# Kernel tuning notes

Hardware: AMD Instinct MI355X
Metric: run time of the kernel (lower is better)

## Reference

```python
import jax, jax.numpy as jnp
import numpy as np

B, S, D, I, L, H, F = 4, 512, 768, 64, 2, 12, 3072
DH = D // H
LN_EPS = 1e-12


def setup_inputs() -> dict:
    key = jax.random.key(0)
    ks = jax.random.split(key, 24)
    nrm = lambda k, sh, s=0.02: jax.random.normal(k, sh, jnp.float32) * s
    return {
        'hs0': nrm(ks[0], (B, S, D), 1.0),
        'hs1': nrm(ks[1], (B, S, D), 1.0),
        'hs2': nrm(ks[2], (B, S, D), 1.0),
        'Wq': nrm(ks[3], (L, D, D)), 'bq': jnp.zeros((L, D), jnp.float32),
        'Wk': nrm(ks[4], (L, D, D)), 'bk': jnp.zeros((L, D), jnp.float32),
        'Wv': nrm(ks[5], (L, D, D)), 'bv': jnp.zeros((L, D), jnp.float32),
        'Wo': nrm(ks[6], (L, D, D)), 'bo': jnp.zeros((L, D), jnp.float32),
        'ln1_g': jnp.ones((L, D), jnp.float32), 'ln1_b': jnp.zeros((L, D), jnp.float32),
        'W1': nrm(ks[7], (L, D, F)), 'b1': jnp.zeros((L, F), jnp.float32),
        'W2': nrm(ks[8], (L, F, D)), 'b2': jnp.zeros((L, D), jnp.float32),
        'ln2_g': jnp.ones((L, D), jnp.float32), 'ln2_b': jnp.zeros((L, D), jnp.float32),
        'zero_context': nrm(ks[9], (D,), 1.0),
        'ck2tok_mask': jax.random.uniform(ks[10], (B, I, S)) > 0.7,  # True = token excluded from span
        'span_size_ids': jax.random.randint(ks[11], (B, I), 0, 10),
    }


def _ln(x, g, b):
    m = jnp.mean(x, axis=-1, keepdims=True)
    v = jnp.mean((x - m) ** 2, axis=-1, keepdims=True)
    return (x - m) * jax.lax.rsqrt(v + LN_EPS) * g + b


def _forward(hs0, hs1, Wq, bq, Wk, bk, Wv, bv, Wo, bo, ln1_g, ln1_b,
             W1, b1, W2, b2, ln2_g, ln2_b, zero_context, mask):
    # mask: [B,I,S] bool, True = excluded token
    zero_indic = jnp.all(mask, axis=-1)                 # [B,I] spans with no valid token
    mask = mask & ~zero_indic[:, :, None]               # unmask degenerate rows (replaced at end)
    # masked max pooling (init aggregation) -- [B,I,S,D] intermediate, traffic-bound
    pooled = jnp.max(jnp.where(mask[..., None], -jnp.inf, hs0[:, None, :, :]), axis=2)  # [B,I,D]
    ext = (mask.astype(jnp.float32) * -10000.0)[:, None, :, :]  # [B,1,I,S] extended attn mask
    q = pooled
    hs_list = (hs0, hs1)
    inv_sqrt_dh = np.float32(1.0 / np.sqrt(DH))
    for i in range(L):
        hs = hs_list[i]
        qh = (q @ Wq[i] + bq[i]).reshape(B, I, H, DH).transpose(0, 2, 1, 3)   # [B,H,I,DH]
        kh = (hs @ Wk[i] + bk[i]).reshape(B, S, H, DH).transpose(0, 2, 1, 3)  # [B,H,S,DH]
        vh = (hs @ Wv[i] + bv[i]).reshape(B, S, H, DH).transpose(0, 2, 1, 3)
        scores = jnp.einsum('bhid,bhsd->bhis', qh, kh) * inv_sqrt_dh + ext
        attn = jax.nn.softmax(scores, axis=-1)
        ctx = jnp.einsum('bhis,bhsd->bhid', attn, vh).transpose(0, 2, 1, 3).reshape(B, I, D)
        q = _ln(q + ctx @ Wo[i] + bo[i], ln1_g[i], ln1_b[i])
        ffn = jax.nn.gelu(q @ W1[i] + b1[i], approximate=False) @ W2[i] + b2[i]
        q = _ln(q + ffn, ln2_g[i], ln2_b[i])
    # zero-context substitution for empty spans
    return jnp.where(zero_indic[..., None], zero_context, q)


def reference(hs0, hs1, hs2, Wq, bq, Wk, bk, Wv, bv, Wo, bo, ln1_g, ln1_b,
              W1, b1, W2, b2, ln2_g, ln2_b, zero_context, ck2tok_mask, span_size_ids):
    # hs2 is the last entry of the (num_layers+1) slice; query layers 0..L-1 attend hs0..hs1.
    # span_size_ids unused since use_init_size_emb=False.
    del hs2, span_size_ids
    return _forward(hs0, hs1, Wq, bq, Wk, bk, Wv, bv, Wo, bo, ln1_g, ln1_b,
                    W1, b1, W2, b2, ln2_g, ln2_b, zero_context, ck2tok_mask)
```

## Files before the change

kernel.cpp:

```cpp
#include <hip/hip_runtime.h>
#include <hip/hip_bf16.h>
#include <math.h>

#define BB 4
#define SS 512
#define DD 768
#define II 64
#define LL 2
#define HH 12
#define FF 3072

using short8 = __attribute__((ext_vector_type(8))) short;
using f32x4  = __attribute__((ext_vector_type(4))) float;

__device__ __forceinline__ unsigned short f2bf(float x) {
  return __builtin_bit_cast(unsigned short, __float2bfloat16(x));
}

__device__ __forceinline__ void gload_lds16(const void* g, void* l) {
  __builtin_amdgcn_global_load_lds((const __attribute__((address_space(1))) unsigned int*)g,
                                   (__attribute__((address_space(3))) unsigned int*)l, 16, 0, 0);
}

__global__ __launch_bounds__(256) void castmask_kernel(
    const float* __restrict__ hs0, const float* __restrict__ hs1,
    unsigned short* __restrict__ hsb0, unsigned short* __restrict__ hsb1,
    const int* __restrict__ mask, int* __restrict__ zi,
    unsigned long long* __restrict__ pmask, unsigned char* __restrict__ emask) {
  int id = blockIdx.x, t = threadIdx.x;
  if (id < 1536) {
    int idx = id * 256 + t;
    float4 va = ((const float4*)hs0)[idx];
    float4 vb = ((const float4*)hs1)[idx];
    union { unsigned short u[4]; uint2 v; } pa, pb;
    pa.u[0] = f2bf(va.x); pa.u[1] = f2bf(va.y); pa.u[2] = f2bf(va.z); pa.u[3] = f2bf(va.w);
    pb.u[0] = f2bf(vb.x); pb.u[1] = f2bf(vb.y); pb.u[2] = f2bf(vb.z); pb.u[3] = f2bf(vb.w);
    ((uint2*)hsb0)[idx] = pa.v;
    ((uint2*)hsb1)[idx] = pb.v;
  } else {
    int bi = id - 1536;
    int w = t >> 6;
    const int* mrow = mask + (size_t)bi * SS;
    int m0v = mrow[t], m1v = mrow[t + 256];
    int incl = (m0v == 0) | (m1v == 0);
    int any = __syncthreads_or(incl);
    int z = !any;
    unsigned long long w0 = __ballot(z || (m0v == 0));
    unsigned long long w1 = __ballot(z || (m1v == 0));
    if ((t & 63) == 0) {
      pmask[bi * 8 + w] = w0;
      pmask[bi * 8 + 4 + w] = w1;
      if (t == 0) zi[bi] = z;
    }
    emask[(size_t)bi * SS + t] = (unsigned char)((!z) & (m0v != 0));
    emask[(size_t)bi * SS + t + 256] = (unsigned char)((!z) & (m1v != 0));
  }
}

struct TC { const float* s[6]; };

__global__ __launch_bounds__(256) void tcast_kernel(TC src, unsigned short* __restrict__ WT4,
                                                    unsigned short* __restrict__ W1T,
                                                    unsigned short* __restrict__ W2T) {
  __shared__ float smem[8192];
  int id = blockIdx.x, t = threadIdx.x;
  const float* Ws; unsigned short* WTs; int K, N, k0, n0;
  if (id < 576) {
    int z = id / 72, rem = id - z * 72;
    int widx = z >> 1, l = z & 1;
    Ws = src.s[widx] + (size_t)l * DD * DD;
    WTs = WT4 + ((size_t)widx * 2 + l) * DD * DD;
    K = DD; N = DD; k0 = (rem / 6) * 64; n0 = (rem % 6) * 128;
  } else if (id < 1152) {
    int j = id - 576, l = j / 288, rem = j - l * 288;
    Ws = src.s[4] + (size_t)l * DD * FF;
    WTs = W1T + (size_t)l * FF * DD;
    K = DD; N = FF; k0 = (rem / 24) * 64; n0 = (rem % 24) * 128;
  } else {
    int j = id - 1152, l = j / 288, rem = j - l * 288;
    Ws = src.s[5] + (size_t)l * FF * DD;
    WTs = W2T + (size_t)l * DD * FF;
    K = FF; N = DD; k0 = (rem / 6) * 64; n0 = (rem % 6) * 128;
  }
  int w = t >> 6, lane = t & 63;
  #pragma unroll
  for (int cc = 0; cc < 8; ++cc) {
    int c = w * 8 + cc;
    int row = c * 2 + (lane >> 5);
    int cbyte = (lane & 31) * 16;
    int scb = cbyte ^ ((row & 7) << 4);
    gload_lds16((const char*)(Ws + (size_t)(k0 + row) * N + n0) + scb, (char*)smem + c * 1024);
  }
  __syncthreads();
  int n = t >> 1, kh = t & 1;
  union { unsigned short u[32]; uint4 v4[4]; } pk;
  #pragma unroll
  for (int i = 0; i < 32; ++i) {
    int kl = kh * 32 + i;
    float f = *(const float*)((const char*)smem + kl * 512 + ((n * 4) ^ ((kl & 7) << 4)));
    pk.u[i] = f2bf(f);
  }
  uint4* dst = (uint4*)(WTs + (size_t)(n0 + n) * K + k0 + kh * 32);
  dst[0] = pk.v4[0]; dst[1] = pk.v4[1]; dst[2] = pk.v4[2]; dst[3] = pk.v4[3];
}

#define PCH 32
__global__ __launch_bounds__(256) void pool2_kernel(const float* __restrict__ hs0,
                                                    const unsigned char* __restrict__ emask,
                                                    float* __restrict__ qf,
                                                    unsigned short* __restrict__ qb) {
  __shared__ float hsb[2][PCH * 256];
  __shared__ unsigned char em[4 * SS];
  int id = blockIdx.x;
  int ig = id & 15, bdz = id >> 4;
  int dz = bdz % 3, b = bdz / 3;
  int t = threadIdx.x, w = t >> 6, lane = t & 63;
  if (w == 0) {
    const char* esrc = (const char*)emask + ((size_t)(b * II + ig * 4)) * SS;
    gload_lds16(esrc + lane * 16, (char*)em);
    gload_lds16(esrc + 1024 + lane * 16, (char*)em + 1024);
  }
  const float* hb = hs0 + (size_t)(b * SS) * DD + dz * 256;
  auto STAGE = [&](int buf, int it) {
    #pragma unroll
    for (int cc = 0; cc < 8; ++cc) {
      int c = w * 8 + cc;
      gload_lds16((const char*)(hb + (size_t)(it * PCH + c) * DD) + lane * 16,
                  (char*)hsb[buf] + c * 1024);
    }
  };
  STAGE(0, 0);
  float m0 = -3.4e38f, m1 = -3.4e38f, m2 = -3.4e38f, m3 = -3.4e38f;
  const float NEG = -__builtin_inff();
  int cur = 0;
  for (int it = 0; it < 16; ++it) {
    if (it + 1 < 16) {
      STAGE(cur ^ 1, it + 1);
      asm volatile("s_waitcnt vmcnt(8)" ::: "memory");
    } else {
      asm volatile("s_waitcnt vmcnt(0)" ::: "memory");
    }
    __builtin_amdgcn_s_barrier();
    const float* hp = hsb[cur];
    const unsigned char* e0 = em + it * PCH;
    const unsigned char* e1 = e0 + SS;
    const unsigned char* e2 = e1 + SS;
    const unsigned char* e3 = e2 + SS;
    #pragma unroll 8
    for (int s = 0; s < PCH; ++s) {
      float v = hp[s * 256 + t];
      m0 = fmaxf(m0, v + (e0[s] ? NEG : 0.0f));
      m1 = fmaxf(m1, v + (e1[s] ? NEG : 0.0f));
      m2 = fmaxf(m2, v + (e2[s] ? NEG : 0.0f));
      m3 = fmaxf(m3, v + (e3[s] ? NEG : 0.0f));
    }
    __builtin_amdgcn_s_barrier();
    cur ^= 1;
  }
  size_t r0 = (size_t)(b * II + ig * 4) * DD + dz * 256 + t;
  qf[r0] = m0;          qb[r0] = f2bf(m0);
  qf[r0 + DD] = m1;     qb[r0 + DD] = f2bf(m1);
  qf[r0 + 2 * DD] = m2; qb[r0 + 2 * DD] = f2bf(m2);
  qf[r0 + 3 * DD] = m3; qb[r0 + 3 * DD] = f2bf(m3);
}

struct GB { const unsigned short* A; const unsigned short* Bt; const float* bias; void* C;
            int M; int N; int rowbias; };

template <int GELU, int OUTBF>
__global__ __launch_bounds__(256) void gemm_nt(GB g0, GB g1, GB g2, GB g3, int K) {
  __shared__ unsigned short Al[2][128 * 64];
  __shared__ unsigned short Bl[2][128 * 64];
  GB g = (blockIdx.z == 0) ? g0 : (blockIdx.z == 1) ? g1 : (blockIdx.z == 2) ? g2 : g3;
  int bm = blockIdx.x, bn = blockIdx.y;
  if (blockIdx.z & 1) { bm = blockIdx.y; bn = blockIdx.x; }
  if (bm * 128 >= g.M) return;
  int t = threadIdx.x, w = t >> 6, lane = t & 63;
  int hi = lane >> 4, lo = lane & 15;
  int wr = w >> 1, wc = w & 1;
  f32x4 acc[4][4] = {};
  const char* Abase = (const char*)g.A + (size_t)(bm * 128) * (size_t)K * 2;
  const char* Bbase = (const char*)g.Bt + (size_t)(bn * 128) * (size_t)K * 2;
  int rowbytes = K * 2;
  int KT = K >> 6;
  auto STAGE = [&](int buf, int kt) {
    int k0b = kt * 128;
    #pragma unroll
    for (int c = 0; c < 4; ++c) {
      int base = (c * 4 + w) << 10;
      int o = base + lane * 16;
      int row = o >> 7, cb = o & 127;
      int scb = cb ^ ((row & 7) << 4);
      gload_lds16(Abase + (size_t)row * rowbytes + (k0b + scb), (char*)Al[buf] + base);
      gload_lds16(Bbase + (size_t)row * rowbytes + (k0b + scb), (char*)Bl[buf] + base);
    }
  };
  STAGE(0, 0);
  asm volatile("s_waitcnt vmcnt(0)" ::: "memory");
  __builtin_amdgcn_s_barrier();
  int cur = 0;
  for (int kt = 0; kt < KT; ++kt) {
    if (kt + 1 < KT) STAGE(cur ^ 1, kt + 1);
    #pragma unroll
    for (int kk = 0; kk < 2; ++kk) {
      short8 av[4], bv_[4];
      #pragma unroll
      for (int mi = 0; mi < 4; ++mi) {
        int r = wr * 64 + mi * 16 + lo;
        av[mi] = *(const short8*)((const char*)Al[cur] + r * 128 + ((kk * 64 + hi * 16) ^ ((r & 7) << 4)));
      }
      #pragma unroll
      for (int ni = 0; ni < 4; ++ni) {
        int r = wc * 64 + ni * 16 + lo;
        bv_[ni] = *(const short8*)((const char*)Bl[cur] + r * 128 + ((kk * 64 + hi * 16) ^ ((r & 7) << 4)));
      }
      #pragma unroll
      for (int mi = 0; mi < 4; ++mi)
        #pragma unroll
        for (int ni = 0; ni < 4; ++ni)
          acc[mi][ni] = __builtin_amdgcn_mfma_f32_16x16x32_bf16(av[mi], bv_[ni], acc[mi][ni], 0, 0, 0);
    }
    if (kt + 1 < KT) {
      asm volatile("s_waitcnt vmcnt(0)" ::: "memory");
      __builtin_amdgcn_s_barrier();
      cur ^= 1;
    }
  }
  int mbase = bm * 128 + wr * 64;
  int nbase = bn * 128 + wc * 64;
  #pragma unroll
  for (int mi = 0; mi < 4; ++mi)
    #pragma unroll
    for (int ni = 0; ni < 4; ++ni)
      #pragma unroll
      for (int r = 0; r < 4; ++r) {
        int gm = mbase + mi * 16 + hi * 4 + r;
        int gn = nbase + ni * 16 + lo;
        float v = acc[mi][ni][r] + (g.rowbias ? g.bias[gm] : g.bias[gn]);
        if (GELU) v = 0.5f * v * (1.0f + erff(v * 0.70710678118654752f));
        if (OUTBF) ((unsigned short*)g.C)[(size_t)gm * g.N + gn] = f2bf(v);
        else       ((float*)g.C)[(size_t)gm * g.N + gn] = v;
      }
}

template <int GELU, int OUTBF, int PARTIAL>
__global__ __launch_bounds__(256) void gemm_sk(GB g, int K, int kLen) {
  __shared__ unsigned short Al[2][64 * 64];
  __shared__ unsigned short Bl[2][64 * 64];
  int bm = blockIdx.x, bn = blockIdx.y, bz = blockIdx.z;
  int t = threadIdx.x, w = t >> 6, lane = t & 63;
  int hi = lane >> 4, lo = lane & 15;
  int wr = w >> 1, wc = w & 1;
  f32x4 acc[2][2] = {};
  size_t rb = (size_t)K * 2;
  const char* Abase = (const char*)g.A + (size_t)(bm * 64) * rb + (size_t)bz * kLen * 2;
  const char* Bbase = (const char*)g.Bt + (size_t)(bn * 64) * rb + (size_t)bz * kLen * 2;
  int KT = kLen >> 6;
  auto STAGE = [&](int buf, int kt) {
    int k0b = kt * 128;
    #pragma unroll
    for (int c = 0; c < 2; ++c) {
      int base = (c * 4 + w) << 10;
      int o = base + lane * 16;
      int row = o >> 7, cb = o & 127;
      int scb = cb ^ ((row & 7) << 4);
      gload_lds16(Abase + (size_t)row * rb + (k0b + scb), (char*)Al[buf] + base);
      gload_lds16(Bbase + (size_t)row * rb + (k0b + scb), (char*)Bl[buf] + base);
    }
  };
  STAGE(0, 0);
  asm volatile("s_waitcnt vmcnt(0)" ::: "memory");
  __builtin_amdgcn_s_barrier();
  int cur = 0;
  for (int kt = 0; kt < KT; ++kt) {
    if (kt + 1 < KT) STAGE(cur ^ 1, kt + 1);
    #pragma unroll
    for (int kk = 0; kk < 2; ++kk) {
      short8 av[2], bv_[2];
      #pragma unroll
      for (int mi = 0; mi < 2; ++mi) {
        int r = wr * 32 + mi * 16 + lo;
        av[mi] = *(const short8*)((const char*)Al[cur] + r * 128 + ((kk * 64 + hi * 16) ^ ((r & 7) << 4)));
      }
      #pragma unroll
      for (int ni = 0; ni < 2; ++ni) {
        int r = wc * 32 + ni * 16 + lo;
        bv_[ni] = *(const short8*)((const char*)Bl[cur] + r * 128 + ((kk * 64 + hi * 16) ^ ((r & 7) << 4)));
      }
      #pragma unroll
      for (int mi = 0; mi < 2; ++mi)
        #pragma unroll
        for (int ni = 0; ni < 2; ++ni)
          acc[mi][ni] = __builtin_amdgcn_mfma_f32_16x16x32_bf16(av[mi], bv_[ni], acc[mi][ni], 0, 0, 0);
    }
    if (kt + 1 < KT) {
      asm volatile("s_waitcnt vmcnt(0)" ::: "memory");
      __builtin_amdgcn_s_barrier();
      cur ^= 1;
    }
  }
  int mbase = bm * 64 + wr * 32;
  int nbase = bn * 64 + wc * 32;
  #pragma unroll
  for (int mi = 0; mi < 2; ++mi)
    #pragma unroll
    for (int ni = 0; ni < 2; ++ni)
      #pragma unroll
      for (int r = 0; r < 4; ++r) {
        int gm = mbase + mi * 16 + hi * 4 + r;
        int gn = nbase + ni * 16 + lo;
        if (PARTIAL) {
          ((float*)g.C)[((size_t)bz * g.M + gm) * g.N + gn] = acc[mi][ni][r];
        } else {
          float v = acc[mi][ni][r] + g.bias[gn];
          if (GELU) v = 0.5f * v * (1.0f + erff(v * 0.70710678118654752f));
          if (OUTBF) ((unsigned short*)g.C)[(size_t)gm * g.N + gn] = f2bf(v);
          else       ((float*)g.C)[(size_t)gm * g.N + gn] = v;
        }
      }
}

#define ATTN_LDS 145664
__global__ __launch_bounds__(256) void attn_kernel(
    const unsigned short* __restrict__ qbuf, const unsigned short* __restrict__ WqTl,
    const float* __restrict__ bql, const unsigned short* __restrict__ khb,
    const unsigned short* __restrict__ vTall, const unsigned long long* __restrict__ pmask,
    unsigned short* __restrict__ ctx) {
  extern __shared__ char lds[];
  char* Qd = lds;
  char* KP = lds + 8192;
  char* Vd = lds + 8192 + 65536;
  unsigned long long* pm = (unsigned long long*)(lds + 139264);
  float* red  = (float*)(lds + 143360);
  float* red2 = (float*)(lds + 144384);
  float* rnv  = (float*)(lds + 145408);
  int bh = blockIdx.x;
  int b = bh / HH, h = bh - b * HH;
  int t = threadIdx.x, w = t >> 6, l = t & 63, hi = l >> 4, lo = l & 15;
  int o16 = l * 16, ro = o16 >> 7, cb = o16 & 127;

  const char* vsrc = (const char*)vTall + (size_t)(h * 64) * 4096 + (size_t)b * 1024;
  #pragma unroll
  for (int rr = 0; rr < 16; ++rr) {
    int rv = w * 16 + rr;
    gload_lds16(vsrc + (size_t)rv * 4096 + ((l * 16) ^ ((rv & 7) << 4)), Vd + rv * 1024);
  }
  if (w == 0) {
    const char* psrc = (const char*)pmask + (size_t)b * 4096;
    #pragma unroll
    for (int c = 0; c < 4; ++c) gload_lds16(psrc + c * 1024 + l * 16, (char*)pm + c * 1024);
  }

  const char* Aq = (const char*)qbuf + (size_t)(b * II) * 1536;
  const char* Bq = (const char*)WqTl + (size_t)(h * 64) * 1536;
  f32x4 qacc[4] = {};
  #pragma unroll
  for (int cc = 0; cc < 2; ++cc) {
    int ch = w * 2 + cc, row = ch * 8 + ro;
    int scb = cb ^ ((row & 7) << 4);
    gload_lds16(Aq + (size_t)row * 1536 + scb, KP + ch * 1024);
    gload_lds16(Bq + (size_t)row * 1536 + scb, KP + 8192 + ch * 1024);
  }
  __syncthreads();
  for (int kt = 0; kt < 12; ++kt) {
    int cur = (kt & 1) * 16384;
    if (kt < 11) {
      int nxt = ((kt + 1) & 1) * 16384;
      int kb = (kt + 1) * 128;
      #pragma unroll
      for (int cc = 0; cc < 2; ++cc) {
        int ch = w * 2 + cc, row = ch * 8 + ro;
        int scb = kb + (cb ^ ((row & 7) << 4));
        gload_lds16(Aq + (size_t)row * 1536 + scb, KP + nxt + ch * 1024);
        gload_lds16(Bq + (size_t)row * 1536 + scb, KP + nxt + 8192 + ch * 1024);
      }
    }
    #pragma unroll
    for (int kk = 0; kk < 2; ++kk) {
      int ra = w * 16 + lo;
      short8 av = *(const short8*)(KP + cur + ra * 128 + ((kk * 64 + hi * 16) ^ ((ra & 7) << 4)));
      #pragma unroll
      for (int ni = 0; ni < 4; ++ni) {
        int rb2 = ni * 16 + lo;
        short8 bv = *(const short8*)(KP + cur + 8192 + rb2 * 128 + ((kk * 64 + hi * 16) ^ ((rb2 & 7) << 4)));
        qacc[ni] = __builtin_amdgcn_mfma_f32_16x16x32_bf16(av, bv, qacc[ni], 0, 0, 0);
      }
    }
    __syncthreads();
  }
  #pragma unroll
  for (int ni = 0; ni < 4; ++ni)
    #pragma unroll
    for (int r = 0; r < 4; ++r) {
      int row = w * 16 + hi * 4 + r, col = ni * 16 + lo;
      float v = qacc[ni][r] + bql[h * 64 + col];
      *(unsigned short*)(Qd + row * 128 + ((col * 2) ^ ((row & 7) << 4))) = f2bf(v);
    }
  const char* Ks = (const char*)khb + (size_t)(b * SS) * 1536 + h * 128;
  #pragma unroll
  for (int cc = 0; cc < 16; ++cc) {
    int ch = w * 16 + cc, row = ch * 8 + ro;
    int scb = cb ^ ((row & 7) << 4);
    gload_lds16(Ks + (size_t)row * 1536 + scb, KP + ch * 1024);
  }
  __syncthreads();

  f32x4 acc[4][8] = {};
  #pragma unroll
  for (int kk = 0; kk < 2; ++kk) {
    short8 av[4];
    #pragma unroll
    for (int mi = 0; mi < 4; ++mi) {
      int ra = mi * 16 + lo;
      av[mi] = *(const short8*)(Qd + ra * 128 + ((kk * 64 + hi * 16) ^ ((ra & 7) << 4)));
    }
    #pragma unroll
    for (int ni = 0; ni < 8; ++ni) {
      int rk = w * 128 + ni * 16 + lo;
      short8 bv = *(const short8*)(KP + rk * 128 + ((kk * 64 + hi * 16) ^ ((rk & 7) << 4)));
      #pragma unroll
      for (int mi = 0; mi < 4; ++mi)
        acc[mi][ni] = __builtin_amdgcn_mfma_f32_16x16x32_bf16(av[mi], bv, acc[mi][ni], 0, 0, 0);
    }
  }
  #pragma unroll
  for (int mi = 0; mi < 4; ++mi)
    #pragma unroll
    for (int r = 0; r < 4; ++r) {
      float m = acc[mi][0][r];
      #pragma unroll
      for (int ni = 1; ni < 8; ++ni) m = fmaxf(m, acc[mi][ni][r]);
      #pragma unroll
      for (int xm = 1; xm <= 8; xm <<= 1) m = fmaxf(m, __shfl_xor(m, xm));
      if (lo == 0) red[(mi * 16 + hi * 4 + r) * 4 + w] = m;
    }
  __syncthreads();
  #pragma unroll
  for (int mi = 0; mi < 4; ++mi)
    #pragma unroll
    for (int r = 0; r < 4; ++r) {
      int row = mi * 16 + hi * 4 + r;
      float4 rm4 = *(const float4*)&red[row * 4];
      float gm = fmaxf(fmaxf(rm4.x, rm4.y), fmaxf(rm4.z, rm4.w));
      unsigned long long w0 = pm[row * 8 + w * 2 + 0];
      unsigned long long w1 = pm[row * 8 + w * 2 + 1];
      float s = 0.f;
      #pragma unroll
      for (int ni = 0; ni < 8; ++ni) {
        int sl = ni * 16 + lo;
        unsigned long long word = (sl < 64) ? w0 : w1;
        float in = ((word >> (sl & 63)) & 1ull) ? 1.0f : 0.0f;
        float e = __expf((acc[mi][ni][r] - gm) * 0.125f) * in;
        s += e;
        int sbyte = w * 256 + ni * 32 + lo * 2;
        *(unsigned short*)(KP + row * 1024 + (sbyte ^ ((row & 7) << 4))) = f2bf(e);
      }
      #pragma unroll
      for (int xm = 1; xm <= 8; xm <<= 1) s += __shfl_xor(s, xm);
      if (lo == 0) red2[row * 4 + w] = s;
    }
  __syncthreads();
  if (w == 0 && lo == 0) {
    #pragma unroll
    for (int mi = 0; mi < 4; ++mi)
      #pragma unroll
      for (int r = 0; r < 4; ++r) {
        int row = mi * 16 + hi * 4 + r;
        float4 s4 = *(const float4*)&red2[row * 4];
        rnv[row] = 1.0f / ((s4.x + s4.y) + (s4.z + s4.w));
      }
  }
  __syncthreads();
  f32x4 pacc[4] = {};
  for (int kk = 0; kk < 16; ++kk) {
    int rv = w * 16 + lo;
    short8 bv = *(const short8*)(Vd + rv * 1024 + ((kk * 64 + hi * 16) ^ ((rv & 7) << 4)));
    #pragma unroll
    for (int mi = 0; mi < 4; ++mi) {
      int ra = mi * 16 + lo;
      short8 av = *(const short8*)(KP + ra * 1024 + ((kk * 64 + hi * 16) ^ ((ra & 7) << 4)));
      pacc[mi] = __builtin_amdgcn_mfma_f32_16x16x32_bf16(av, bv, pacc[mi], 0, 0, 0);
    }
  }
  #pragma unroll
  for (int mi = 0; mi < 4; ++mi)
    #pragma unroll
    for (int r = 0; r < 4; ++r) {
      int row = mi * 16 + hi * 4 + r;
      ctx[(size_t)(b * II + row) * DD + h * 64 + w * 16 + lo] = f2bf(pacc[mi][r] * rnv[row]);
    }
}

template <int FINAL, int NP>
__global__ __launch_bounds__(256) void ln_kernel(const float* __restrict__ x, const float* __restrict__ y,
                                                 const float* __restrict__ gb,
                                                 const float* __restrict__ g, const float* __restrict__ bb,
                                                 float* __restrict__ qf, unsigned short* __restrict__ qb,
                                                 const int* __restrict__ zi, const float* __restrict__ zc,
                                                 float* __restrict__ out) {
  __shared__ float r1[4], r2[4];
  const int MN = BB * II * DD;
  int r = blockIdx.x, t = threadIdx.x;
  size_t o = (size_t)r * DD;
  float v0 = x[o + t] + gb[t];
  float v1 = x[o + t + 256] + gb[t + 256];
  float v2 = x[o + t + 512] + gb[t + 512];
  #pragma unroll
  for (int p = 0; p < NP; ++p) {
    size_t po = (size_t)p * MN + o;
    v0 += y[po + t];
    v1 += y[po + t + 256];
    v2 += y[po + t + 512];
  }
  float s = v0 + v1 + v2, ss = v0 * v0 + v1 * v1 + v2 * v2;
  #pragma unroll
  for (int o2 = 32; o2; o2 >>= 1) { s += __shfl_xor(s, o2); ss += __shfl_xor(ss, o2); }
  if ((t & 63) == 0) { r1[t >> 6] = s; r2[t >> 6] = ss; }
  __syncthreads();
  s = r1[0] + r1[1] + r1[2] + r1[3];
  ss = r2[0] + r2[1] + r2[2] + r2[3];
  float mean = s * (1.0f / DD);
  float var = ss * (1.0f / DD) - mean * mean;
  float inv = rsqrtf(var + 1e-12f);
  float w0 = (v0 - mean) * inv * g[t] + bb[t];
  float w1 = (v1 - mean) * inv * g[t + 256] + bb[t + 256];
  float w2 = (v2 - mean) * inv * g[t + 512] + bb[t + 512];
  if (FINAL) {
    int z = zi[r];
    out[o + t] = z ? zc[t] : w0;
    out[o + t + 256] = z ? zc[t + 256] : w1;
    out[o + t + 512] = z ? zc[t + 512] : w2;
  } else {
    qf[o + t] = w0; qf[o + t + 256] = w1; qf[o + t + 512] = w2;
    qb[o + t] = f2bf(w0); qb[o + t + 256] = f2bf(w1); qb[o + t + 512] = f2bf(w2);
  }
}

extern "C" void kernel_launch(void* const* d_in, const int* in_sizes, int n_in,
                              void* d_out, int out_size, void* d_ws, size_t ws_size,
                              hipStream_t stream) {
  (void)in_sizes; (void)n_in; (void)out_size; (void)ws_size;
  const float* hs0 = (const float*)d_in[0];
  const float* hs1 = (const float*)d_in[1];
  const float* Wq  = (const float*)d_in[3];
  const float* bq  = (const float*)d_in[4];
  const float* Wk  = (const float*)d_in[5];
  const float* bk  = (const float*)d_in[6];
  const float* Wv  = (const float*)d_in[7];
  const float* bv  = (const float*)d_in[8];
  const float* Wo  = (const float*)d_in[9];
  const float* bo  = (const float*)d_in[10];
  const float* ln1g = (const float*)d_in[11];
  const float* ln1b = (const float*)d_in[12];
  const float* W1  = (const float*)d_in[13];
  const float* b1  = (const float*)d_in[14];
  const float* W2  = (const float*)d_in[15];
  const float* b2  = (const float*)d_in[16];
  const float* ln2g = (const float*)d_in[17];
  const float* ln2b = (const float*)d_in[18];
  const float* zc  = (const float*)d_in[19];
  const int*   mask = (const int*)d_in[20];

  char* ws = (char*)d_ws;
  size_t off = 0;
  auto alloc = [&](size_t bytes) { size_t o = off; off += (bytes + 255) & ~(size_t)255; return o; };

  unsigned short* WT4 = (unsigned short*)(ws + alloc((size_t)4 * LL * DD * DD * 2));
  unsigned short* W1T = (unsigned short*)(ws + alloc((size_t)LL * FF * DD * 2));
  unsigned short* W2T = (unsigned short*)(ws + alloc((size_t)LL * DD * FF * 2));
  unsigned short* hsb = (unsigned short*)(ws + alloc((size_t)2 * BB * SS * DD * 2));
  float*          qf  = (float*)(ws + alloc((size_t)BB * II * DD * 4));
  unsigned short* qb  = (unsigned short*)(ws + alloc((size_t)BB * II * DD * 2));
  unsigned short* khb = (unsigned short*)(ws + alloc((size_t)LL * BB * SS * DD * 2));
  unsigned short* vTall = (unsigned short*)(ws + alloc((size_t)LL * DD * BB * SS * 2));
  unsigned short* ctxb = (unsigned short*)(ws + alloc((size_t)BB * II * DD * 2));
  float*          att_o = (float*)(ws + alloc((size_t)2 * BB * II * DD * 4));
  unsigned short* ffh = (unsigned short*)(ws + alloc((size_t)BB * II * FF * 2));
  float*          ffo = (float*)(ws + alloc((size_t)4 * BB * II * DD * 4));
  unsigned long long* pmask = (unsigned long long*)(ws + alloc((size_t)BB * II * 8 * 8));
  unsigned char*  emask = (unsigned char*)(ws + alloc((size_t)BB * II * SS));
  int*            zib = (int*)(ws + alloc((size_t)BB * II * 4));

  unsigned short* WqT = WT4 + 0 * (size_t)LL * DD * DD;
  unsigned short* WkT = WT4 + 1 * (size_t)LL * DD * DD;
  unsigned short* WvT = WT4 + 2 * (size_t)LL * DD * DD;
  unsigned short* WoT = WT4 + 3 * (size_t)LL * DD * DD;

  (void)hipFuncSetAttribute((const void*)attn_kernel,
                            hipFuncAttributeMaxDynamicSharedMemorySize, ATTN_LDS);

  castmask_kernel<<<1536 + 256, 256, 0, stream>>>(hs0, hs1, hsb, hsb + (size_t)BB * SS * DD,
                                                  mask, zib, pmask, emask);
  TC tc = { { Wq, Wk, Wv, Wo, W1, W2 } };
  tcast_kernel<<<1728, 256, 0, stream>>>(tc, WT4, W1T, W2T);
  pool2_kernel<<<192, 256, 0, stream>>>(hs0, emask, qf, qb);

  {
    const unsigned short* h0 = hsb;
    const unsigned short* h1 = hsb + (size_t)BB * SS * DD;
    GB gK0 = { h0, WkT, bk, khb, BB * SS, DD, 0 };
    GB gV0 = { WvT, h0, bv, vTall, DD, BB * SS, 1 };
    GB gK1 = { h1, WkT + (size_t)DD * DD, bk + DD, khb + (size_t)BB * SS * DD, BB * SS, DD, 0 };
    GB gV1 = { WvT + (size_t)DD * DD, h1, bv + DD, vTall + (size_t)DD * BB * SS, DD, BB * SS, 1 };
    gemm_nt<0, 1><<<dim3(16, 6, 4), 256, 0, stream>>>(gK0, gV0, gK1, gV1, DD);
  }

  for (int l = 0; l < LL; ++l) {
    const unsigned short* khl = khb + (size_t)l * BB * SS * DD;
    const unsigned short* vTl = vTall + (size_t)l * DD * BB * SS;
    attn_kernel<<<dim3(BB * HH), 256, ATTN_LDS, stream>>>(
        qb, WqT + (size_t)l * DD * DD, bq + l * DD, khl, vTl, pmask, ctxb);
    GB gO = { ctxb, WoT + (size_t)l * DD * DD, nullptr, att_o, BB * II, DD, 0 };
    gemm_sk<0, 0, 1><<<dim3(4, 12, 2), 256, 0, stream>>>(gO, DD, DD / 2);
    ln_kernel<0, 2><<<BB * II, 256, 0, stream>>>(qf, att_o, bo + l * DD,
                                                 ln1g + l * DD, ln1b + l * DD, qf, qb,
                                                 nullptr, nullptr, nullptr);
    GB gF1 = { qb, W1T + (size_t)l * FF * DD, b1 + l * FF, ffh, BB * II, FF, 0 };
    gemm_sk<1, 1, 0><<<dim3(4, FF / 64, 1), 256, 0, stream>>>(gF1, DD, DD);
    GB gF2 = { ffh, W2T + (size_t)l * DD * FF, nullptr, ffo, BB * II, DD, 0 };
    gemm_sk<0, 0, 1><<<dim3(4, 12, 4), 256, 0, stream>>>(gF2, FF, FF / 4);
    if (l == 0)
      ln_kernel<0, 4><<<BB * II, 256, 0, stream>>>(qf, ffo, b2 + l * DD,
                                                   ln2g + l * DD, ln2b + l * DD, qf, qb,
                                                   nullptr, nullptr, nullptr);
    else
      ln_kernel<1, 4><<<BB * II, 256, 0, stream>>>(qf, ffo, b2 + l * DD,
                                                   ln2g + l * DD, ln2b + l * DD, nullptr, nullptr,
                                                   zib, zc, (float*)d_out);
  }
}
```

Measured before the change: 199.2 us.

## Rewrite masked max pooling with one block per span row and direct loads

The pooling kernel drops the LDS double-buffered staging of hs0 that computed four span rows per block. It now launches one block per (batch, span, 256-column slice), 768 blocks instead of 192. Each block turns its mask row into additive -inf values in shared memory and reads hs0 columns straight from global memory into eight independent max accumulators. The goal is more parallelism and less synchronisation, but each hs0 column is now read by four times as many blocks, which leans on L2 to absorb the extra traffic.

```diff
diff --git a/kernel.cpp b/kernel.cpp
--- a/kernel.cpp
+++ b/kernel.cpp
@@ -104,64 +104,36 @@
   dst[0] = pk.v4[0]; dst[1] = pk.v4[1]; dst[2] = pk.v4[2]; dst[3] = pk.v4[3];
 }
 
-#define PCH 32
-__global__ __launch_bounds__(256) void pool2_kernel(const float* __restrict__ hs0,
+__global__ __launch_bounds__(256) void pool3_kernel(const float* __restrict__ hs0,
                                                     const unsigned char* __restrict__ emask,
                                                     float* __restrict__ qf,
                                                     unsigned short* __restrict__ qb) {
-  __shared__ float hsb[2][PCH * 256];
-  __shared__ unsigned char em[4 * SS];
-  int id = blockIdx.x;
-  int ig = id & 15, bdz = id >> 4;
-  int dz = bdz % 3, b = bdz / 3;
-  int t = threadIdx.x, w = t >> 6, lane = t & 63;
-  if (w == 0) {
-    const char* esrc = (const char*)emask + ((size_t)(b * II + ig * 4)) * SS;
-    gload_lds16(esrc + lane * 16, (char*)em);
-    gload_lds16(esrc + 1024 + lane * 16, (char*)em + 1024);
-  }
-  const float* hb = hs0 + (size_t)(b * SS) * DD + dz * 256;
-  auto STAGE = [&](int buf, int it) {
-    #pragma unroll
-    for (int cc = 0; cc < 8; ++cc) {
-      int c = w * 8 + cc;
-      gload_lds16((const char*)(hb + (size_t)(it * PCH + c) * DD) + lane * 16,
-                  (char*)hsb[buf] + c * 1024);
-    }
-  };
-  STAGE(0, 0);
-  float m0 = -3.4e38f, m1 = -3.4e38f, m2 = -3.4e38f, m3 = -3.4e38f;
-  const float NEG = -__builtin_inff();
-  int cur = 0;
-  for (int it = 0; it < 16; ++it) {
-    if (it + 1 < 16) {
-      STAGE(cur ^ 1, it + 1);
-      asm volatile("s_waitcnt vmcnt(8)" ::: "memory");
-    } else {
-      asm volatile("s_waitcnt vmcnt(0)" ::: "memory");
-    }
-    __builtin_amdgcn_s_barrier();
-    const float* hp = hsb[cur];
-    const unsigned char* e0 = em + it * PCH;
-    const unsigned char* e1 = e0 + SS;
-    const unsigned char* e2 = e1 + SS;
-    const unsigned char* e3 = e2 + SS;
-    #pragma unroll 8
-    for (int s = 0; s < PCH; ++s) {
-      float v = hp[s * 256 + t];
-      m0 = fmaxf(m0, v + (e0[s] ? NEG : 0.0f));
-      m1 = fmaxf(m1, v + (e1[s] ? NEG : 0.0f));
-      m2 = fmaxf(m2, v + (e2[s] ? NEG : 0.0f));
-      m3 = fmaxf(m3, v + (e3[s] ? NEG : 0.0f));
-    }
-    __builtin_amdgcn_s_barrier();
-    cur ^= 1;
-  }
-  size_t r0 = (size_t)(b * II + ig * 4) * DD + dz * 256 + t;
-  qf[r0] = m0;          qb[r0] = f2bf(m0);
-  qf[r0 + DD] = m1;     qb[r0 + DD] = f2bf(m1);
-  qf[r0 + 2 * DD] = m2; qb[r0 + 2 * DD] = f2bf(m2);
-  qf[r0 + 3 * DD] = m3; qb[r0 + 3 * DD] = f2bf(m3);
+  __shared__ float eadd[SS];
+  int bi = blockIdx.x, dz = blockIdx.y;
+  int b = bi >> 6, t = threadIdx.x;
+  if (t < 128) {
+    uchar4 e4 = ((const uchar4*)(emask + (size_t)bi * SS))[t];
+    const float NEG = -__builtin_inff();
+    eadd[t * 4 + 0] = e4.x ? NEG : 0.0f;
+    eadd[t * 4 + 1] = e4.y ? NEG : 0.0f;
+    eadd[t * 4 + 2] = e4.z ? NEG : 0.0f;
+    eadd[t * 4 + 3] = e4.w ? NEG : 0.0f;
+  }
+  __syncthreads();
+  const float* hb = hs0 + (size_t)b * SS * DD + dz * 256 + t;
+  float m[8];
+  #pragma unroll
+  for (int j = 0; j < 8; ++j) m[j] = -3.4e38f;
+  for (int s0 = 0; s0 < SS; s0 += 8) {
+    #pragma unroll
+    for (int j = 0; j < 8; ++j)
+      m[j] = fmaxf(m[j], hb[(size_t)(s0 + j) * DD] + eadd[s0 + j]);
+  }
+  float mm = fmaxf(fmaxf(fmaxf(m[0], m[1]), fmaxf(m[2], m[3])),
+                   fmaxf(fmaxf(m[4], m[5]), fmaxf(m[6], m[7])));
+  size_t o = (size_t)bi * DD + dz * 256 + t;
+  qf[o] = mm;
+  qb[o] = f2bf(mm);
 }
 
 struct GB { const unsigned short* A; const unsigned short* Bt; const float* bias; void* C;
@@ -593,7 +565,7 @@
                                                   mask, zib, pmask, emask);
   TC tc = { { Wq, Wk, Wv, Wo, W1, W2 } };
   tcast_kernel<<<1728, 256, 0, stream>>>(tc, WT4, W1T, W2T);
-  pool2_kernel<<<192, 256, 0, stream>>>(hs0, emask, qf, qb);
+  pool3_kernel<<<dim3(BB * II, 3), 256, 0, stream>>>(hs0, emask, qf, qb);
 
   {
     const unsigned short* h0 = hsb;
```

New measurement: 183.1 us. -8.1%, faster.
